# Optimization experiments

Hardware: AMD Instinct MI355X
Metric: run time of the kernel (lower is better)

Reference implementation:

```python
import jax, jax.numpy as jnp
import numpy as np

NUM_HEADS = 16

def setup_inputs() -> dict:
    key = jax.random.key(0)
    ks = jax.random.split(key, 8)
    L, S, N, E = 2048, 2048, 2, 1024
    return {
        "query": jax.random.normal(ks[0], (L, N, E), jnp.float32),
        "key": jax.random.normal(ks[1], (S, N, E), jnp.float32),
        "value": jax.random.normal(ks[2], (S, N, E), jnp.float32),
        "in_proj_weight": jax.random.normal(ks[3], (3 * E, E), jnp.float32) * (E ** -0.5),
        "in_proj_bias": jax.random.normal(ks[4], (3 * E,), jnp.float32) * 0.01,
        "out_proj_weight": jax.random.normal(ks[5], (E, E), jnp.float32) * (E ** -0.5),
        "out_proj_bias": jax.random.normal(ks[6], (E,), jnp.float32) * 0.01,
        "rel_bias": jax.random.normal(ks[7], (NUM_HEADS, 2 * S - 1), jnp.float32) * 0.02,
    }


def reference(query, key, value, in_proj_weight, in_proj_bias,
              out_proj_weight, out_proj_bias, rel_bias):
    L, N, E = query.shape
    S = key.shape[0]
    H = NUM_HEADS
    D = E // H
    scaling = D ** -0.5

    # in-projection: F.linear(x, W, b) = x @ W.T + b, with W split into q/k/v rows
    wq, wk, wv = jnp.split(in_proj_weight, 3, axis=0)
    bq, bk, bv = jnp.split(in_proj_bias, 3, axis=0)
    q = (query @ wq.T + bq) * scaling          # [L,N,E]
    k = key @ wk.T + bk                        # [S,N,E]
    v = value @ wv.T + bv                      # [S,N,E]

    q = q.reshape(L, N, H, D)
    k = k.reshape(S, N, H, D)
    v = v.reshape(S, N, H, D)

    # attention scores [N,H,L,S]
    scores = jnp.einsum("lnhd,snhd->nhls", q, k)

    # relative-position bias: bias[h,i,j] = rel_bias[h, (i - j) + S - 1]
    rel_idx = jnp.arange(L)[:, None] - jnp.arange(S)[None, :] + (S - 1)  # [L,S]
    bias = rel_bias[:, rel_idx]                # [H,L,S]
    scores = scores + bias[None, :, :, :]

    attn = jax.nn.softmax(scores, axis=-1)     # [N,H,L,S]

    out = jnp.einsum("nhls,snhd->lnhd", attn, v).reshape(L, N, E)
    out = out @ out_proj_weight.T + out_proj_bias  # [L,N,E]
    return out
```

## Files before the change

### kernel.cpp

```cpp
#include <hip/hip_runtime.h>
#include <hip/hip_bf16.h>


typedef __attribute__((ext_vector_type(8))) short bf16x8;
typedef __attribute__((ext_vector_type(4))) float f32x4;
typedef __attribute__((ext_vector_type(16))) float f32x16;
typedef __attribute__((ext_vector_type(4))) unsigned int u32x4;

#define LOG2E 1.4426950408889634f

__device__ __forceinline__ unsigned short f2bf(float x) {
  unsigned u = __float_as_uint(x);
  u += 0x7fffu + ((u >> 16) & 1u);
  return (unsigned short)(u >> 16);
}

__device__ __forceinline__ void gld_lds16(const void* g, void* l) {
  __builtin_amdgcn_global_load_lds(
      (const __attribute__((address_space(1))) unsigned int*)g,
      (__attribute__((address_space(3))) unsigned int*)l,
      16, 0, 0);
}

__global__ __launch_bounds__(256) void cvt_qkv(const float* __restrict__ q,
                                               const float* __restrict__ k,
                                               const float* __restrict__ v,
                                               unsigned short* __restrict__ dst) {
  const int z = blockIdx.y;
  const float* src = (z == 0) ? q : (z == 1) ? k : v;
  int i = blockIdx.x * 256 + threadIdx.x;
  float4 vv = reinterpret_cast<const float4*>(src)[i];
  ushort4 o;
  o.x = f2bf(vv.x); o.y = f2bf(vv.y); o.z = f2bf(vv.z); o.w = f2bf(vv.w);
  reinterpret_cast<ushort4*>(dst + (size_t)z * 4194304)[i] = o;
}

__global__ __launch_bounds__(256) void cvt_w(const float* __restrict__ w_in,
                                             const float* __restrict__ w_out,
                                             unsigned short* __restrict__ wIn,
                                             unsigned short* __restrict__ wOut) {
  int i = blockIdx.x * 256 + threadIdx.x;
  if (i < 786432) {
    float scale = (i < 262144) ? 0.125f * LOG2E : 1.0f;
    float4 vv = reinterpret_cast<const float4*>(w_in)[i];
    ushort4 o;
    o.x = f2bf(vv.x * scale); o.y = f2bf(vv.y * scale);
    o.z = f2bf(vv.z * scale); o.w = f2bf(vv.w * scale);
    reinterpret_cast<ushort4*>(wIn)[i] = o;
  } else {
    int j = i - 786432;
    float4 vv = reinterpret_cast<const float4*>(w_out)[j];
    ushort4 o;
    o.x = f2bf(vv.x); o.y = f2bf(vv.y); o.z = f2bf(vv.z); o.w = f2bf(vv.w);
    reinterpret_cast<ushort4*>(wOut)[j] = o;
  }
}

template<int OUT_F32, int QKV>
__global__ __launch_bounds__(256) void gemm_nt(const unsigned short* __restrict__ Abase,
                                               const unsigned short* __restrict__ Wbase,
                                               const float* __restrict__ biasBase,
                                               void* __restrict__ outBase) {
  const int K = 1024, Nout = 1024;
  __shared__ __attribute__((aligned(16))) unsigned short As[2][128 * 32];
  __shared__ __attribute__((aligned(16))) unsigned short Bs[2][128 * 32];

  const int tid = threadIdx.x;
  const int l = tid & 63, w = tid >> 6;
  const int lane15 = tid & 15, lhi = (tid >> 4) & 3;
  const int Mbase = blockIdx.y * 128, Nbase = blockIdx.x * 128;
  const int rb = (w >> 1) * 64, cb = (w & 1) * 64;

  const unsigned short* A = Abase;
  const unsigned short* W = Wbase;
  const float* bias = biasBase;
  float biasScale = 1.0f;
  unsigned short* outU = (unsigned short*)outBase;
  float* outF = (float*)outBase;
  if (QKV) {
    const int z = blockIdx.z;
    A    += (size_t)z * 4194304;
    W    += (size_t)z * 1048576;
    bias += z * 1024;
    outU += (size_t)z * 4194304;
    if (z == 0) biasScale = 0.125f * LOG2E;
  }

  auto stage = [&](int kt, int buf) {
#pragma unroll
    for (int i = 0; i < 2; ++i) {
      int u = (i * 4 + w) * 64 + l;
      int row = u >> 2, slot = u & 3;
      int ks = slot ^ ((row >> 1) & 3);
      gld_lds16(A + (size_t)(Mbase + row) * K + kt * 32 + ks * 8,
                &As[buf][(i * 4 + w) * 512]);
      gld_lds16(W + (size_t)(Nbase + row) * K + kt * 32 + ks * 8,
                &Bs[buf][(i * 4 + w) * 512]);
    }
  };

  f32x4 acc[4][4] = {};
  stage(0, 0);
  const int NK = 32;
  for (int kt = 0; kt < NK; ++kt) {
    __syncthreads();
    if (kt + 1 < NK) stage(kt + 1, (kt + 1) & 1);
    const int buf = kt & 1;
    bf16x8 a[4], b[4];
#pragma unroll
    for (int m = 0; m < 4; ++m) {
      int row = rb + m * 16 + lane15;
      a[m] = *(const bf16x8*)&As[buf][row * 32 + (lhi ^ ((row >> 1) & 3)) * 8];
      int col = cb + m * 16 + lane15;
      b[m] = *(const bf16x8*)&Bs[buf][col * 32 + (lhi ^ ((col >> 1) & 3)) * 8];
    }
#pragma unroll
    for (int m = 0; m < 4; ++m)
#pragma unroll
      for (int nt = 0; nt < 4; ++nt)
        acc[m][nt] = __builtin_amdgcn_mfma_f32_16x16x32_bf16(a[m], b[nt], acc[m][nt], 0, 0, 0);
  }

  float bv[4];
#pragma unroll
  for (int nt = 0; nt < 4; ++nt)
    bv[nt] = bias[Nbase + cb + nt * 16 + lane15] * biasScale;
#pragma unroll
  for (int m = 0; m < 4; ++m)
#pragma unroll
    for (int nt = 0; nt < 4; ++nt)
#pragma unroll
      for (int r = 0; r < 4; ++r) {
        float v = acc[m][nt][r] + bv[nt];
        size_t idx = (size_t)(Mbase + rb + m * 16 + lhi * 4 + r) * Nout +
                     (Nbase + cb + nt * 16 + lane15);
        if (OUT_F32) outF[idx] = v;
        else         outU[idx] = f2bf(v);
      }
}

__global__ __launch_bounds__(256) void vtrans(const unsigned short* __restrict__ vP,
                                              unsigned short* __restrict__ vT) {
  __shared__ unsigned short t_lds[64][66];
  const int tid = threadIdx.x;
  const int st = blockIdx.x, nh = blockIdx.y;
  const int n = nh >> 4, h = nh & 15;
  const int sb = st * 64;
#pragma unroll
  for (int r = 0; r < 2; ++r) {
    int idx = tid + r * 256;
    int row = idx >> 3, ch = idx & 7;
    bf16x8 v = *(const bf16x8*)(vP + (size_t)((sb + row) * 2 + n) * 1024 + h * 64 + ch * 8);
#pragma unroll
    for (int j = 0; j < 8; ++j) t_lds[row][ch * 8 + j] = (unsigned short)v[j];
  }
  __syncthreads();
#pragma unroll
  for (int r = 0; r < 2; ++r) {
    int idx = tid + r * 256;
    int d = idx >> 3, sc = idx & 7;
    bf16x8 o;
#pragma unroll
    for (int j = 0; j < 8; ++j) o[j] = (short)t_lds[sc * 8 + j][d];
    *(bf16x8*)(vT + (size_t)(nh * 64 + d) * 2048 + sb + sc * 8) = o;
  }
}

__global__ __launch_bounds__(256) void attn(const unsigned short* __restrict__ qP,
                                            const unsigned short* __restrict__ kP,
                                            const unsigned short* __restrict__ vT,
                                            const float* __restrict__ rel_bias,
                                            unsigned short* __restrict__ attnout) {
  __shared__ __attribute__((aligned(16))) float bias4[4 * 2180];
  __shared__ __attribute__((aligned(16))) unsigned short Ks[2][4096];
  __shared__ __attribute__((aligned(16))) unsigned short Vs[2][4096];

  const int tid = threadIdx.x;
  const int l = tid & 63, w = tid >> 6;
  const int l31 = tid & 31, lh5 = (tid >> 5) & 1;
  const int qt = blockIdx.x, nh = blockIdx.y;
  const int n = nh >> 4, h = nh & 15;
  const int qb = qt * 128;
  const int wq = w * 32;
  const int lloc = wq + l31;

#pragma unroll
  for (int m = 0; m < 4; ++m)
    for (int i = tid; i < 2176; i += 256) {
      int src = qb + i + m;
      bias4[m * 2180 + i] = (src <= 4094) ? rel_bias[h * 4095 + src] * LOG2E : 0.f;
    }

  bf16x8 qf[4];
  {
    const unsigned short* qrow = qP + (size_t)((qb + lloc) * 2 + n) * 1024 + h * 64;
#pragma unroll
    for (int m16 = 0; m16 < 4; ++m16)
      qf[m16] = *(const bf16x8*)(qrow + m16 * 16 + lh5 * 8);
  }

  const short one_bf = (short)0x3F80;
  bf16x8 ones = {one_bf, one_bf, one_bf, one_bf, one_bf, one_bf, one_bf, one_bf};

  f32x16 o0 = {}, o1 = {}, osum = {};

  auto stage = [&](int kt, int buf) {
#pragma unroll
    for (int i = 0; i < 2; ++i) {
      int u = (i * 4 + w) * 64 + l;
      int row = u >> 3, slot = u & 7;
      int ks = slot ^ (row & 7);
      gld_lds16(kP + (size_t)((kt * 64 + row) * 2 + n) * 1024 + h * 64 + ks * 8,
                &Ks[buf][(i * 4 + w) * 512]);
      gld_lds16(vT + (size_t)(nh * 64 + row) * 2048 + kt * 64 + ks * 8,
                &Vs[buf][(i * 4 + w) * 512]);
    }
  };

  stage(0, 0);
  for (int kt = 0; kt < 32; ++kt) {
    __syncthreads();
    if (kt + 1 < 32) stage(kt + 1, (kt + 1) & 1);
    const int buf = kt & 1;

#pragma unroll
    for (int sb = 0; sb < 2; ++sb) {
      const int srow = sb * 32 + l31;
      bf16x8 kf[4];
#pragma unroll
      for (int m16 = 0; m16 < 4; ++m16)
        kf[m16] = *(const bf16x8*)&Ks[buf][srow * 64 + (((m16 * 2 + lh5) ^ (srow & 7)) * 8)];

      f32x16 c;
#pragma unroll
      for (int rg = 0; rg < 4; ++rg) {
        int a = lloc + 2047 - (kt * 64 + sb * 32 + rg * 8 + lh5 * 4) - 3;
        const float4 f4 = *(const float4*)&bias4[(a & 3) * 2180 + (a & ~3)];
        c[rg * 4 + 0] = f4.w; c[rg * 4 + 1] = f4.z;
        c[rg * 4 + 2] = f4.y; c[rg * 4 + 3] = f4.x;
      }

#pragma unroll
      for (int m16 = 0; m16 < 4; ++m16)
        c = __builtin_amdgcn_mfma_f32_32x32x16_bf16(kf[m16], qf[m16], c, 0, 0, 0);

      float p[16];
#pragma unroll
      for (int i = 0; i < 16; ++i) p[i] = exp2f(c[i]);

      unsigned pk0[4], pk1[4];
#pragma unroll
      for (int rg = 0; rg < 4; ++rg) {
        asm("v_cvt_pk_bf16_f32 %0, %1, %2" : "=v"(pk0[rg]) : "v"(p[rg * 4 + 0]), "v"(p[rg * 4 + 1]));
        asm("v_cvt_pk_bf16_f32 %0, %1, %2" : "=v"(pk1[rg]) : "v"(p[rg * 4 + 2]), "v"(p[rg * 4 + 3]));
      }

#pragma unroll
      for (int t = 0; t < 2; ++t) {
        unsigned x0 = pk0[t * 2 + 0], y0 = pk0[t * 2 + 1];
        unsigned x1 = pk1[t * 2 + 0], y1 = pk1[t * 2 + 1];
        asm("v_permlane32_swap_b32 %0, %1" : "+v"(x0), "+v"(y0));
        asm("v_permlane32_swap_b32 %0, %1" : "+v"(x1), "+v"(y1));
        u32x4 pu; pu[0] = x0; pu[1] = x1; pu[2] = y0; pu[3] = y1;
        bf16x8 pa = __builtin_bit_cast(bf16x8, pu);
        const int tb = sb * 2 + t;
#pragma unroll
        for (int dn = 0; dn < 2; ++dn) {
          int drow = dn * 32 + l31;
          bf16x8 vf = *(const bf16x8*)&Vs[buf][drow * 64 + (((tb * 2 + lh5) ^ (drow & 7)) * 8)];
          if (dn == 0) o0 = __builtin_amdgcn_mfma_f32_32x32x16_bf16(pa, vf, o0, 0, 0, 0);
          else         o1 = __builtin_amdgcn_mfma_f32_32x32x16_bf16(pa, vf, o1, 0, 0, 0);
        }
        osum = __builtin_amdgcn_mfma_f32_32x32x16_bf16(pa, ones, osum, 0, 0, 0);
      }
    }
  }

#pragma unroll
  for (int reg = 0; reg < 16; ++reg) {
    float inv = 1.0f / osum[reg];
    int lrow = qb + wq + (reg & 3) + 8 * (reg >> 2) + 4 * lh5;
    size_t base = (size_t)(lrow * 2 + n) * 1024 + h * 64 + l31;
    attnout[base]      = f2bf(o0[reg] * inv);
    attnout[base + 32] = f2bf(o1[reg] * inv);
  }
}

extern "C" void kernel_launch(void* const* d_in, const int* in_sizes, int n_in,
                              void* d_out, int out_size, void* d_ws, size_t ws_size,
                              hipStream_t stream) {
  (void)in_sizes; (void)n_in; (void)out_size; (void)ws_size;
  const float* query = (const float*)d_in[0];
  const float* key   = (const float*)d_in[1];
  const float* value = (const float*)d_in[2];
  const float* w_in  = (const float*)d_in[3];
  const float* b_in  = (const float*)d_in[4];
  const float* w_out = (const float*)d_in[5];
  const float* b_out = (const float*)d_in[6];
  const float* rel_b = (const float*)d_in[7];

  unsigned short* ws   = (unsigned short*)d_ws;
  unsigned short* qkvA = ws;
  unsigned short* wIn  = ws + 12582912;
  unsigned short* wOut = ws + 15728640;
  unsigned short* qP   = ws + 16777216;
  unsigned short* vT   = ws + 29360128;
  unsigned short* attnout = qkvA;

  dim3 gC(4096, 3);
  cvt_qkv<<<gC, 256, 0, stream>>>(query, key, value, qkvA);
  cvt_w<<<4096, 256, 0, stream>>>(w_in, w_out, wIn, wOut);

  dim3 gQKV(8, 32, 3);
  gemm_nt<0, 1><<<gQKV, 256, 0, stream>>>(qkvA, wIn, b_in, qP);

  dim3 g32(32, 32);
  vtrans<<<g32, 256, 0, stream>>>(qP + 2 * 4194304, vT);
  dim3 gA(16, 32);
  attn<<<gA, 256, 0, stream>>>(qP, qP + 4194304, vT, rel_b, attnout);

  dim3 gOUT(8, 32, 1);
  gemm_nt<1, 0><<<gOUT, 256, 0, stream>>>(attnout, wOut, b_out, d_out);
}
```

Measured before the change: 271.2 us.

## Store relative bias as bf16 in LDS, remap block order, use raw v_exp

Stores the four shifted copies of the relative-position bias in LDS as packed bf16 instead of fp32. This halves the per-tile LDS reads and the bias footprint, and the values are unpacked with shifts and masks. The grid index is remapped so neighbouring blocks cover different heads and batches of the same query tile, which should change L2 locality. exp2f is replaced with the raw v_exp_f32 instruction to skip range handling. Risks are reduced bias precision and the loss of denormal or edge handling in exp.

```diff
diff --git a/kernel.cpp b/kernel.cpp
--- a/kernel.cpp
+++ b/kernel.cpp
@@ -171,25 +171,32 @@
                                             const unsigned short* __restrict__ vT,
                                             const float* __restrict__ rel_bias,
                                             unsigned short* __restrict__ attnout) {
-  __shared__ __attribute__((aligned(16))) float bias4[4 * 2180];
+  __shared__ __attribute__((aligned(16))) unsigned short bias4[4 * 2208];
   __shared__ __attribute__((aligned(16))) unsigned short Ks[2][4096];
   __shared__ __attribute__((aligned(16))) unsigned short Vs[2][4096];
 
   const int tid = threadIdx.x;
   const int l = tid & 63, w = tid >> 6;
   const int l31 = tid & 31, lh5 = (tid >> 5) & 1;
-  const int qt = blockIdx.x, nh = blockIdx.y;
+  const int bid = blockIdx.y * 16 + blockIdx.x;
+  const int qt = bid >> 5;
+  const int nh = (bid & 7) * 4 + ((bid >> 3) & 3);
   const int n = nh >> 4, h = nh & 15;
   const int qb = qt * 128;
   const int wq = w * 32;
   const int lloc = wq + l31;
 
-#pragma unroll
-  for (int m = 0; m < 4; ++m)
-    for (int i = tid; i < 2176; i += 256) {
-      int src = qb + i + m;
-      bias4[m * 2180 + i] = (src <= 4094) ? rel_bias[h * 4095 + src] * LOG2E : 0.f;
-    }
+  for (int i2 = tid; i2 < 1104; i2 += 256) {
+#pragma unroll
+    for (int m = 0; m < 4; ++m) {
+      int s0 = qb + 2 * i2 + m;
+      float f0 = (s0 <= 4094) ? rel_bias[h * 4095 + s0] * LOG2E : 0.f;
+      float f1 = (s0 + 1 <= 4094) ? rel_bias[h * 4095 + s0 + 1] * LOG2E : 0.f;
+      unsigned pk;
+      asm("v_cvt_pk_bf16_f32 %0, %1, %2" : "=v"(pk) : "v"(f0), "v"(f1));
+      *(unsigned*)&bias4[m * 2208 + 2 * i2] = pk;
+    }
+  }
 
   bf16x8 qf[4];
   {
@@ -235,9 +242,11 @@
 #pragma unroll
       for (int rg = 0; rg < 4; ++rg) {
         int a = lloc + 2047 - (kt * 64 + sb * 32 + rg * 8 + lh5 * 4) - 3;
-        const float4 f4 = *(const float4*)&bias4[(a & 3) * 2180 + (a & ~3)];
-        c[rg * 4 + 0] = f4.w; c[rg * 4 + 1] = f4.z;
-        c[rg * 4 + 2] = f4.y; c[rg * 4 + 3] = f4.x;
+        const uint2 dd = *(const uint2*)&bias4[(a & 3) * 2208 + (a & ~3)];
+        c[rg * 4 + 0] = __uint_as_float(dd.y & 0xFFFF0000u);
+        c[rg * 4 + 1] = __uint_as_float(dd.y << 16);
+        c[rg * 4 + 2] = __uint_as_float(dd.x & 0xFFFF0000u);
+        c[rg * 4 + 3] = __uint_as_float(dd.x << 16);
       }
 
 #pragma unroll
@@ -246,7 +255,8 @@
 
       float p[16];
 #pragma unroll
-      for (int i = 0; i < 16; ++i) p[i] = exp2f(c[i]);
+      for (int i = 0; i < 16; ++i)
+        asm("v_exp_f32 %0, %1" : "=v"(p[i]) : "v"(c[i]));
 
       unsigned pk0[4], pk1[4];
 #pragma unroll
```

Result: faster. 243.5 us (-10.2%).

## Interleave QK MFMAs across both key sub-blocks and remap block ids for locality

Applied to the files above, without the earlier changes.

Loads both 32-row K fragments at once and interleaves the two independent QK^T MFMA chains so they can overlap. Raw v_exp_f32 replaces exp2f, and s_setprio is raised around MFMA bursts to favour matrix issue across waves. Block ids are remapped so concurrent blocks group heads differently, and the bias LDS stride is padded to change bank mapping. This costs more VGPRs for the doubled fragments and scores, which may reduce occupancy.

```diff
diff --git a/kernel.cpp b/kernel.cpp
--- a/kernel.cpp
+++ b/kernel.cpp
@@ -8,6 +8,7 @@
 typedef __attribute__((ext_vector_type(4))) unsigned int u32x4;
 
 #define LOG2E 1.4426950408889634f
+#define BSTRIDE 2184
 
 __device__ __forceinline__ unsigned short f2bf(float x) {
   unsigned u = __float_as_uint(x);
@@ -171,25 +172,28 @@
                                             const unsigned short* __restrict__ vT,
                                             const float* __restrict__ rel_bias,
                                             unsigned short* __restrict__ attnout) {
-  __shared__ __attribute__((aligned(16))) float bias4[4 * 2180];
+  __shared__ __attribute__((aligned(16))) float bias4[4 * BSTRIDE];
   __shared__ __attribute__((aligned(16))) unsigned short Ks[2][4096];
   __shared__ __attribute__((aligned(16))) unsigned short Vs[2][4096];
 
   const int tid = threadIdx.x;
   const int l = tid & 63, w = tid >> 6;
   const int l31 = tid & 31, lh5 = (tid >> 5) & 1;
-  const int qt = blockIdx.x, nh = blockIdx.y;
+  const int bid = blockIdx.y * 16 + blockIdx.x;
+  const int qt = bid >> 5;
+  const int nh = (bid & 7) * 4 + ((bid >> 3) & 3);
   const int n = nh >> 4, h = nh & 15;
   const int qb = qt * 128;
   const int wq = w * 32;
   const int lloc = wq + l31;
 
-#pragma unroll
-  for (int m = 0; m < 4; ++m)
-    for (int i = tid; i < 2176; i += 256) {
+  for (int i = tid; i < 2180; i += 256) {
+#pragma unroll
+    for (int m = 0; m < 4; ++m) {
       int src = qb + i + m;
-      bias4[m * 2180 + i] = (src <= 4094) ? rel_bias[h * 4095 + src] * LOG2E : 0.f;
-    }
+      bias4[m * BSTRIDE + i] = (src <= 4094) ? rel_bias[h * 4095 + src] * LOG2E : 0.f;
+    }
+  }
 
   bf16x8 qf[4];
   {
@@ -223,38 +227,50 @@
     if (kt + 1 < 32) stage(kt + 1, (kt + 1) & 1);
     const int buf = kt & 1;
 
+    bf16x8 kf0[4], kf1[4];
+    const int srow0 = l31, srow1 = 32 + l31;
+#pragma unroll
+    for (int m16 = 0; m16 < 4; ++m16) {
+      kf0[m16] = *(const bf16x8*)&Ks[buf][srow0 * 64 + (((m16 * 2 + lh5) ^ (srow0 & 7)) * 8)];
+      kf1[m16] = *(const bf16x8*)&Ks[buf][srow1 * 64 + (((m16 * 2 + lh5) ^ (srow1 & 7)) * 8)];
+    }
+    f32x16 c0, c1;
 #pragma unroll
     for (int sb = 0; sb < 2; ++sb) {
-      const int srow = sb * 32 + l31;
-      bf16x8 kf[4];
-#pragma unroll
-      for (int m16 = 0; m16 < 4; ++m16)
-        kf[m16] = *(const bf16x8*)&Ks[buf][srow * 64 + (((m16 * 2 + lh5) ^ (srow & 7)) * 8)];
-
-      f32x16 c;
 #pragma unroll
       for (int rg = 0; rg < 4; ++rg) {
         int a = lloc + 2047 - (kt * 64 + sb * 32 + rg * 8 + lh5 * 4) - 3;
-        const float4 f4 = *(const float4*)&bias4[(a & 3) * 2180 + (a & ~3)];
+        const float4 f4 = *(const float4*)&bias4[(a & 3) * BSTRIDE + (a & ~3)];
+        f32x16& c = sb ? c1 : c0;
         c[rg * 4 + 0] = f4.w; c[rg * 4 + 1] = f4.z;
         c[rg * 4 + 2] = f4.y; c[rg * 4 + 3] = f4.x;
       }
-
-#pragma unroll
-      for (int m16 = 0; m16 < 4; ++m16)
-        c = __builtin_amdgcn_mfma_f32_32x32x16_bf16(kf[m16], qf[m16], c, 0, 0, 0);
-
-      float p[16];
-#pragma unroll
-      for (int i = 0; i < 16; ++i) p[i] = exp2f(c[i]);
-
+    }
+
+    __builtin_amdgcn_s_setprio(1);
+#pragma unroll
+    for (int m16 = 0; m16 < 4; ++m16) {
+      c0 = __builtin_amdgcn_mfma_f32_32x32x16_bf16(kf0[m16], qf[m16], c0, 0, 0, 0);
+      c1 = __builtin_amdgcn_mfma_f32_32x32x16_bf16(kf1[m16], qf[m16], c1, 0, 0, 0);
+    }
+    __builtin_amdgcn_s_setprio(0);
+
+    float p0[16], p1[16];
+#pragma unroll
+    for (int i = 0; i < 16; ++i) {
+      asm("v_exp_f32 %0, %1" : "=v"(p0[i]) : "v"(c0[i]));
+      asm("v_exp_f32 %0, %1" : "=v"(p1[i]) : "v"(c1[i]));
+    }
+
+#pragma unroll
+    for (int sb = 0; sb < 2; ++sb) {
+      const float* p = sb ? p1 : p0;
       unsigned pk0[4], pk1[4];
 #pragma unroll
       for (int rg = 0; rg < 4; ++rg) {
         asm("v_cvt_pk_bf16_f32 %0, %1, %2" : "=v"(pk0[rg]) : "v"(p[rg * 4 + 0]), "v"(p[rg * 4 + 1]));
         asm("v_cvt_pk_bf16_f32 %0, %1, %2" : "=v"(pk1[rg]) : "v"(p[rg * 4 + 2]), "v"(p[rg * 4 + 3]));
       }
-
 #pragma unroll
       for (int t = 0; t < 2; ++t) {
         unsigned x0 = pk0[t * 2 + 0], y0 = pk0[t * 2 + 1];
@@ -264,14 +280,13 @@
         u32x4 pu; pu[0] = x0; pu[1] = x1; pu[2] = y0; pu[3] = y1;
         bf16x8 pa = __builtin_bit_cast(bf16x8, pu);
         const int tb = sb * 2 + t;
-#pragma unroll
-        for (int dn = 0; dn < 2; ++dn) {
-          int drow = dn * 32 + l31;
-          bf16x8 vf = *(const bf16x8*)&Vs[buf][drow * 64 + (((tb * 2 + lh5) ^ (drow & 7)) * 8)];
-          if (dn == 0) o0 = __builtin_amdgcn_mfma_f32_32x32x16_bf16(pa, vf, o0, 0, 0, 0);
-          else         o1 = __builtin_amdgcn_mfma_f32_32x32x16_bf16(pa, vf, o1, 0, 0, 0);
-        }
+        bf16x8 vf0 = *(const bf16x8*)&Vs[buf][srow0 * 64 + (((tb * 2 + lh5) ^ (srow0 & 7)) * 8)];
+        bf16x8 vf1 = *(const bf16x8*)&Vs[buf][srow1 * 64 + (((tb * 2 + lh5) ^ (srow1 & 7)) * 8)];
+        __builtin_amdgcn_s_setprio(1);
+        o0   = __builtin_amdgcn_mfma_f32_32x32x16_bf16(pa, vf0, o0, 0, 0, 0);
+        o1   = __builtin_amdgcn_mfma_f32_32x32x16_bf16(pa, vf1, o1, 0, 0, 0);
         osum = __builtin_amdgcn_mfma_f32_32x32x16_bf16(pa, ones, osum, 0, 0, 0);
+        __builtin_amdgcn_s_setprio(0);
       }
     }
   }
```

Measured after the change: 257.0 us. 1.06x faster.
